# Kernel optimization log

Measured on AMD Instinct MI355X. Metric: run time of the kernel, lower is better.

Reference implementation:

```python
import jax, jax.numpy as jnp
import numpy as np

B = 8192        # batch
DB = 64         # dim_body
DO = 128        # dim_object
NOBJ = 9        # nb_objects (all connected)
NE = 72         # edges = NOBJ*(NOBJ-1)
DE = 128        # edge feature dim
NISO = 3        # isolated nodes
HID = 256
PHI_OUT = 256
ACT = 32
LOG_SIG_MIN, LOG_SIG_MAX = -20.0, 2.0


def setup_inputs() -> dict:
    key = jax.random.key(0)
    ks = jax.random.split(key, 16)
    s = 0.05
    return {
        "obs": jax.random.normal(ks[0], (B, DB + NOBJ * DO), jnp.float32),
        "edge_features": jax.random.normal(ks[1], (B, NE, DE), jnp.float32),
        # every object id 0..8 appears NE//NOBJ times (static edge targets)
        "edges_to": jnp.tile(jnp.arange(NOBJ, dtype=jnp.int32), NE // NOBJ),
        "isolated_nodes": jax.random.normal(ks[2], (B, NISO, DO), jnp.float32),
        "isolated_nodes_features": jax.random.normal(ks[3], (B, NISO, DE), jnp.float32),
        "W1_phi": jax.random.normal(ks[4], (DB + DO + DE, HID), jnp.float32) * s,
        "b1_phi": jnp.zeros((HID,), jnp.float32),
        "W2_phi": jax.random.normal(ks[5], (HID, PHI_OUT), jnp.float32) * s,
        "b2_phi": jnp.zeros((PHI_OUT,), jnp.float32),
        "W1_rho": jax.random.normal(ks[6], (PHI_OUT, HID), jnp.float32) * s,
        "b1_rho": jnp.zeros((HID,), jnp.float32),
        "Wm": jax.random.normal(ks[7], (HID, ACT), jnp.float32) * s,
        "bm": jnp.zeros((ACT,), jnp.float32),
        "Ws": jax.random.normal(ks[8], (HID, ACT), jnp.float32) * s,
        "bs": jnp.zeros((ACT,), jnp.float32),
    }


def reference(obs, edge_features, edges_to, isolated_nodes, isolated_nodes_features,
              W1_phi, b1_phi, W2_phi, b2_phi, W1_rho, b1_rho, Wm, bm, Ws, bs):
    obs_body = obs[:, :DB]                              # [B, DB]
    obs_objects = obs[:, DB:].reshape(B, NOBJ, DO)      # [B, NOBJ, DO]

    # per-node max over incoming edges (segment-max over static edge targets)
    ef = jnp.transpose(edge_features, (1, 0, 2))        # [NE, B, DE]
    incoming = jax.ops.segment_max(ef, edges_to, num_segments=NOBJ)  # [NOBJ, B, DE]

    body_c = jnp.broadcast_to(obs_body, (NOBJ, B, DB))
    inp_connected = jnp.concatenate(
        [body_c, jnp.transpose(obs_objects, (1, 0, 2)), incoming], axis=-1)

    body_i = jnp.broadcast_to(obs_body, (NISO, B, DB))
    inp_isolated = jnp.concatenate(
        [body_i,
         jnp.transpose(isolated_nodes, (1, 0, 2)),
         jnp.transpose(isolated_nodes_features, (1, 0, 2))], axis=-1)

    inp = jnp.concatenate([inp_connected, inp_isolated], axis=0)  # [NOBJ+NISO, B, DB+DO+DE]

    # phi DeepSet MLP
    h = jax.nn.relu(inp @ W1_phi + b1_phi)
    phi = jax.nn.relu(h @ W2_phi + b2_phi)

    pooled = phi.sum(axis=0)                            # readout='sum' -> [B, PHI_OUT]

    # rho MLP -> (mean, log_std)
    r = jax.nn.relu(pooled @ W1_rho + b1_rho)
    mean = r @ Wm + bm
    log_std = jnp.clip(r @ Ws + bs, LOG_SIG_MIN, LOG_SIG_MAX)
    return mean, log_std
```

## Files before the change

### kernel.cpp

```cpp
#include <hip/hip_runtime.h>
#include <hip/hip_bf16.h>
#include <stdint.h>


#define Bsz   8192
#define OBSW  1216
#define NH    256

typedef unsigned short u16;
typedef unsigned int   u32;

using bf16x8 = __attribute__((ext_vector_type(8))) short;
using f32x4  = __attribute__((ext_vector_type(4))) float;

__device__ u16   g_W1t[256 * 320];
__device__ u16   g_W2t[256 * 256];
__device__ u16   g_Rt [256 * 256];
__device__ u16   g_Wcat[64 * 256];
__device__ float g_pool2[2][Bsz * NH];

__device__ __forceinline__ u16 f2bf(float f) {
  union { float f; u32 i; } v; v.f = f;
  u32 x = v.i;
  x += 0x7fffu + ((x >> 16) & 1u);
  return (u16)(x >> 16);
}
__device__ __forceinline__ uint4 pack8(const float* f) {
  uint4 o;
  o.x = (u32)f2bf(f[0]) | ((u32)f2bf(f[1]) << 16);
  o.y = (u32)f2bf(f[2]) | ((u32)f2bf(f[3]) << 16);
  o.z = (u32)f2bf(f[4]) | ((u32)f2bf(f[5]) << 16);
  o.w = (u32)f2bf(f[6]) | ((u32)f2bf(f[7]) << 16);
  return o;
}
__device__ __forceinline__ void load8f(const float* p, float* f) {
  *(float4*)(f)     = *(const float4*)(p);
  *(float4*)(f + 4) = *(const float4*)(p + 4);
}

__global__ void transpose_cast(const float* __restrict__ in, int dst,
                               int K, int N, int row_off) {
  __shared__ u16 tile[32][33];
  u16* out = (dst == 0) ? g_W1t : (dst == 1) ? g_W2t : (dst == 2) ? g_Rt : g_Wcat;
  int k0 = blockIdx.x * 32, n0 = blockIdx.y * 32;
  int c = threadIdx.x & 31, r0 = threadIdx.x >> 5;
  #pragma unroll
  for (int i = 0; i < 4; i++) {
    int r = r0 + i * 8;
    tile[r][c] = f2bf(in[(size_t)(k0 + r) * N + (n0 + c)]);
  }
  __syncthreads();
  #pragma unroll
  for (int i = 0; i < 4; i++) {
    int r = r0 + i * 8;
    out[(size_t)(n0 + r + row_off) * K + (k0 + c)] = tile[c][r];
  }
}

__device__ __forceinline__ void loadA(
    int n, size_t sb, int sck,
    const float* __restrict__ obs, const float* __restrict__ ef,
    const float* __restrict__ iso, const float* __restrict__ isof,
    float f[4][8]) {
  if (n < 9) {
    const float* po = obs + sb * OBSW + 64 + (size_t)n * 128 + sck;
    load8f(po, f[0]);
    load8f(po + 64, f[1]);
    const float* base = ef + (sb * 72 + n) * 128 + sck;
    load8f(base, f[2]);
    load8f(base + 64, f[3]);
    #pragma unroll
    for (int j = 1; j < 8; j++) {
      float w0[8], w1[8];
      load8f(base + (size_t)j * 1152, w0);
      load8f(base + (size_t)j * 1152 + 64, w1);
      #pragma unroll
      for (int q = 0; q < 8; q++) {
        f[2][q] = fmaxf(f[2][q], w0[q]);
        f[3][q] = fmaxf(f[3][q], w1[q]);
      }
    }
  } else {
    const float* pi = iso  + (sb * 3 + (n - 9)) * 128 + sck;
    const float* pg = isof + (sb * 3 + (n - 9)) * 128 + sck;
    load8f(pi, f[0]); load8f(pi + 64, f[1]);
    load8f(pg, f[2]); load8f(pg + 64, f[3]);
  }
}

__global__ __launch_bounds__(256, 2)
void node_kernel(const float* __restrict__ obs, const float* __restrict__ ef,
                 const float* __restrict__ iso, const float* __restrict__ isof,
                 const float* __restrict__ b1, const float* __restrict__ b2) {
  __shared__ __attribute__((aligned(16))) u16 As[32][328];
  __shared__ __attribute__((aligned(16))) u16 Ht[32][264];
  const int btile = blockIdx.x >> 1;
  const int nhalf = blockIdx.x & 1;
  const int b0 = btile * 32;
  const int tid = threadIdx.x;
  const int wave = tid >> 6, lane = tid & 63;
  const int nw = wave * 64, lrow = lane & 15, quad = lane >> 4;
  const int srow = tid >> 3, sck = (tid & 7) * 8;
  const size_t sb = (size_t)(b0 + srow);

  {
    float fb[8];
    load8f(obs + sb * OBSW + sck, fb);
    *(uint4*)(&As[srow][sck]) = pack8(fb);
    float f[4][8];
    loadA(nhalf * 6, sb, sck, obs, ef, iso, isof, f);
    #pragma unroll
    for (int c = 0; c < 4; c++)
      *(uint4*)(&As[srow][(c + 1) * 64 + sck]) = pack8(f[c]);
  }
  __syncthreads();

  const f32x4 vzero = {0.f, 0.f, 0.f, 0.f};
  f32x4 pool[2][4];
  #pragma unroll
  for (int a = 0; a < 2; a++)
    #pragma unroll
    for (int b = 0; b < 4; b++) pool[a][b] = vzero;

  for (int nn = 0; nn < 6; nn++) {
    const int n = nhalf * 6 + nn;
    f32x4 acc[2][4];
    #pragma unroll
    for (int a = 0; a < 2; a++)
      #pragma unroll
      for (int b = 0; b < 4; b++) acc[a][b] = vzero;

    #pragma unroll
    for (int kc = 0; kc < 10; kc++) {
      const int kk = kc * 32 + quad * 8;
      bf16x8 af0 = *(const bf16x8*)(&As[lrow][kk]);
      bf16x8 af1 = *(const bf16x8*)(&As[16 + lrow][kk]);
      #pragma unroll
      for (int nb = 0; nb < 4; nb++) {
        bf16x8 bq = *(const bf16x8*)(g_W1t + (size_t)(nw + nb * 16 + lrow) * 320 + kk);
        acc[0][nb] = __builtin_amdgcn_mfma_f32_16x16x32_bf16(af0, bq, acc[0][nb], 0, 0, 0);
        acc[1][nb] = __builtin_amdgcn_mfma_f32_16x16x32_bf16(af1, bq, acc[1][nb], 0, 0, 0);
      }
    }

    float fnext[4][8];
    if (nn < 5) loadA(n + 1, sb, sck, obs, ef, iso, isof, fnext);

    #pragma unroll
    for (int nb = 0; nb < 4; nb++) {
      int col = nw + nb * 16 + lrow;
      float bv = b1[col];
      #pragma unroll
      for (int mb = 0; mb < 2; mb++)
        #pragma unroll
        for (int i = 0; i < 4; i++)
          Ht[mb * 16 + quad * 4 + i][col] = f2bf(fmaxf(acc[mb][nb][i] + bv, 0.f));
    }
    __syncthreads();

    if (nn < 5) {
      #pragma unroll
      for (int c = 0; c < 4; c++)
        *(uint4*)(&As[srow][(c + 1) * 64 + sck]) = pack8(fnext[c]);
    }

    #pragma unroll
    for (int a = 0; a < 2; a++)
      #pragma unroll
      for (int b = 0; b < 4; b++) acc[a][b] = vzero;

    #pragma unroll
    for (int kc = 0; kc < 8; kc++) {
      const int kk = kc * 32 + quad * 8;
      bf16x8 af0 = *(const bf16x8*)(&Ht[lrow][kk]);
      bf16x8 af1 = *(const bf16x8*)(&Ht[16 + lrow][kk]);
      #pragma unroll
      for (int nb = 0; nb < 4; nb++) {
        bf16x8 bq = *(const bf16x8*)(g_W2t + (size_t)(nw + nb * 16 + lrow) * 256 + kk);
        acc[0][nb] = __builtin_amdgcn_mfma_f32_16x16x32_bf16(af0, bq, acc[0][nb], 0, 0, 0);
        acc[1][nb] = __builtin_amdgcn_mfma_f32_16x16x32_bf16(af1, bq, acc[1][nb], 0, 0, 0);
      }
    }
    #pragma unroll
    for (int nb = 0; nb < 4; nb++) {
      int col = nw + nb * 16 + lrow;
      float bv = b2[col];
      #pragma unroll
      for (int mb = 0; mb < 2; mb++)
        #pragma unroll
        for (int i = 0; i < 4; i++)
          pool[mb][nb][i] += fmaxf(acc[mb][nb][i] + bv, 0.f);
    }
    __syncthreads();
  }

  float* op = g_pool2[nhalf];
  #pragma unroll
  for (int nb = 0; nb < 4; nb++) {
    int col = nw + nb * 16 + lrow;
    #pragma unroll
    for (int mb = 0; mb < 2; mb++)
      #pragma unroll
      for (int i = 0; i < 4; i++) {
        int row = b0 + mb * 16 + quad * 4 + i;
        op[(size_t)row * NH + col] = pool[mb][nb][i];
      }
  }
}

__global__ __launch_bounds__(256)
void rho_heads(const float* __restrict__ br, const float* __restrict__ bm,
               const float* __restrict__ bs, float* __restrict__ out) {
  __shared__ __attribute__((aligned(16))) u16 As2[32][264];
  const int b0 = blockIdx.x * 32;
  const int tid = threadIdx.x;
  const int wave = tid >> 6, lane = tid & 63;
  const int nw = wave * 64, lrow = lane & 15, quad = lane >> 4;
  const int srow = tid >> 3, sck = (tid & 7) * 8;

  #pragma unroll
  for (int c4 = 0; c4 < 4; c4++) {
    int col = c4 * 64 + sck;
    float f0[8], f1[8];
    load8f(g_pool2[0] + (size_t)(b0 + srow) * NH + col, f0);
    load8f(g_pool2[1] + (size_t)(b0 + srow) * NH + col, f1);
    #pragma unroll
    for (int q = 0; q < 8; q++) f0[q] += f1[q];
    *(uint4*)(&As2[srow][col]) = pack8(f0);
  }
  __syncthreads();

  const f32x4 vzero = {0.f, 0.f, 0.f, 0.f};
  f32x4 acc[2][4];
  #pragma unroll
  for (int a = 0; a < 2; a++)
    #pragma unroll
    for (int b = 0; b < 4; b++) acc[a][b] = vzero;

  #pragma unroll
  for (int kc = 0; kc < 8; kc++) {
    const int kk = kc * 32 + quad * 8;
    bf16x8 af0 = *(const bf16x8*)(&As2[lrow][kk]);
    bf16x8 af1 = *(const bf16x8*)(&As2[16 + lrow][kk]);
    #pragma unroll
    for (int nb = 0; nb < 4; nb++) {
      bf16x8 bq = *(const bf16x8*)(g_Rt + (size_t)(nw + nb * 16 + lrow) * 256 + kk);
      acc[0][nb] = __builtin_amdgcn_mfma_f32_16x16x32_bf16(af0, bq, acc[0][nb], 0, 0, 0);
      acc[1][nb] = __builtin_amdgcn_mfma_f32_16x16x32_bf16(af1, bq, acc[1][nb], 0, 0, 0);
    }
  }
  __syncthreads();

  #pragma unroll
  for (int nb = 0; nb < 4; nb++) {
    int col = nw + nb * 16 + lrow;
    float bv = br[col];
    #pragma unroll
    for (int mb = 0; mb < 2; mb++)
      #pragma unroll
      for (int i = 0; i < 4; i++)
        As2[mb * 16 + quad * 4 + i][col] = f2bf(fmaxf(acc[mb][nb][i] + bv, 0.f));
  }
  __syncthreads();

  f32x4 acc2[2] = {vzero, vzero};
  #pragma unroll
  for (int kc = 0; kc < 8; kc++) {
    const int kk = kc * 32 + quad * 8;
    bf16x8 af0 = *(const bf16x8*)(&As2[lrow][kk]);
    bf16x8 af1 = *(const bf16x8*)(&As2[16 + lrow][kk]);
    bf16x8 bq  = *(const bf16x8*)(g_Wcat + (size_t)(wave * 16 + lrow) * 256 + kk);
    acc2[0] = __builtin_amdgcn_mfma_f32_16x16x32_bf16(af0, bq, acc2[0], 0, 0, 0);
    acc2[1] = __builtin_amdgcn_mfma_f32_16x16x32_bf16(af1, bq, acc2[1], 0, 0, 0);
  }

  int j = wave * 16 + lrow;
  #pragma unroll
  for (int mb = 0; mb < 2; mb++) {
    #pragma unroll
    for (int i = 0; i < 4; i++) {
      int b = b0 + mb * 16 + quad * 4 + i;
      if (j < 32) {
        out[(size_t)b * 32 + j] = acc2[mb][i] + bm[j];
      } else {
        float v = acc2[mb][i] + bs[j - 32];
        v = fminf(fmaxf(v, -20.f), 2.f);
        out[(size_t)Bsz * 32 + (size_t)b * 32 + (j - 32)] = v;
      }
    }
  }
}

extern "C" void kernel_launch(void* const* d_in, const int* in_sizes, int n_in,
                              void* d_out, int out_size, void* d_ws, size_t ws_size,
                              hipStream_t stream) {
  const float* obs  = (const float*)d_in[0];
  const float* ef   = (const float*)d_in[1];
  const float* iso  = (const float*)d_in[3];
  const float* isof = (const float*)d_in[4];
  const float* W1   = (const float*)d_in[5];
  const float* b1   = (const float*)d_in[6];
  const float* W2   = (const float*)d_in[7];
  const float* b2   = (const float*)d_in[8];
  const float* Wr   = (const float*)d_in[9];
  const float* br   = (const float*)d_in[10];
  const float* Wm   = (const float*)d_in[11];
  const float* bm   = (const float*)d_in[12];
  const float* Wsg  = (const float*)d_in[13];
  const float* bs   = (const float*)d_in[14];
  float* out = (float*)d_out;
  (void)d_ws; (void)ws_size;

  transpose_cast<<<dim3(10, 8), 256, 0, stream>>>(W1, 0, 320, 256, 0);
  transpose_cast<<<dim3(8, 8), 256, 0, stream>>>(W2, 1, 256, 256, 0);
  transpose_cast<<<dim3(8, 8), 256, 0, stream>>>(Wr, 2, 256, 256, 0);
  transpose_cast<<<dim3(8, 1), 256, 0, stream>>>(Wm, 3, 256, 32, 0);
  transpose_cast<<<dim3(8, 1), 256, 0, stream>>>(Wsg, 3, 256, 32, 32);

  node_kernel<<<(Bsz / 32) * 2, 256, 0, stream>>>(obs, ef, iso, isof, b1, b2);
  rho_heads<<<Bsz / 32, 256, 0, stream>>>(br, bm, bs, out);
}
```

Baseline: 587.7 us.

## Halve batch tile to 16 rows, double-buffer node inputs, merge weight transposes

Shrinks the node kernel's batch tile from 32 to 16 rows, which doubles the block count and raises occupancy hints to 4 blocks per CU so more memory traffic can be in flight for the bandwidth-bound edge segment-max loads. It also double-buffers the A tile so the next node's inputs are written straight to LDS during the current node's compute, instead of being held in registers. The five weight-transpose launches are merged into one. In exchange, each block loads every W1/W2 B-fragment for half as many rows, doubling weight traffic from L2 per row, and each wave's MFMA work per fragment load is halved.

```diff
diff --git a/kernel.cpp b/kernel.cpp
--- a/kernel.cpp
+++ b/kernel.cpp
@@ -38,11 +38,18 @@
   *(float4*)(f + 4) = *(const float4*)(p + 4);
 }
 
-__global__ void transpose_cast(const float* __restrict__ in, int dst,
-                               int K, int N, int row_off) {
+__global__ __launch_bounds__(256)
+void transpose_all(const float* __restrict__ W1, const float* __restrict__ W2,
+                   const float* __restrict__ Wr, const float* __restrict__ Wm,
+                   const float* __restrict__ Wsg) {
   __shared__ u16 tile[32][33];
-  u16* out = (dst == 0) ? g_W1t : (dst == 1) ? g_W2t : (dst == 2) ? g_Rt : g_Wcat;
-  int k0 = blockIdx.x * 32, n0 = blockIdx.y * 32;
+  int bx = blockIdx.x;
+  const float* in; u16* out; int K, N, row_off = 0, k0, n0;
+  if (bx < 80)       { in = W1;  out = g_W1t;  K = 320; N = 256; k0 = (bx % 10) * 32; n0 = (bx / 10) * 32; }
+  else if (bx < 144) { bx -= 80;  in = W2;  out = g_W2t;  K = 256; N = 256; k0 = (bx & 7) * 32; n0 = (bx >> 3) * 32; }
+  else if (bx < 208) { bx -= 144; in = Wr;  out = g_Rt;   K = 256; N = 256; k0 = (bx & 7) * 32; n0 = (bx >> 3) * 32; }
+  else if (bx < 216) { bx -= 208; in = Wm;  out = g_Wcat; K = 256; N = 32;  k0 = bx * 32; n0 = 0; }
+  else               { bx -= 216; in = Wsg; out = g_Wcat; K = 256; N = 32;  k0 = bx * 32; n0 = 0; row_off = 32; }
   int c = threadIdx.x & 31, r0 = threadIdx.x >> 5;
   #pragma unroll
   for (int i = 0; i < 4; i++) {
@@ -57,128 +64,109 @@
   }
 }
 
-__device__ __forceinline__ void loadA(
-    int n, size_t sb, int sck,
+__device__ __forceinline__ void loadA16(
+    int n, size_t rb, int sck,
     const float* __restrict__ obs, const float* __restrict__ ef,
     const float* __restrict__ iso, const float* __restrict__ isof,
-    float f[4][8]) {
+    float f[2][8]) {
   if (n < 9) {
-    const float* po = obs + sb * OBSW + 64 + (size_t)n * 128 + sck;
-    load8f(po, f[0]);
-    load8f(po + 64, f[1]);
-    const float* base = ef + (sb * 72 + n) * 128 + sck;
-    load8f(base, f[2]);
-    load8f(base + 64, f[3]);
+    load8f(obs + rb * OBSW + 64 + (size_t)n * 128 + sck, f[0]);
+    const float* base = ef + (rb * 72 + n) * 128 + sck;
+    load8f(base, f[1]);
     #pragma unroll
     for (int j = 1; j < 8; j++) {
-      float w0[8], w1[8];
-      load8f(base + (size_t)j * 1152, w0);
-      load8f(base + (size_t)j * 1152 + 64, w1);
-      #pragma unroll
-      for (int q = 0; q < 8; q++) {
-        f[2][q] = fmaxf(f[2][q], w0[q]);
-        f[3][q] = fmaxf(f[3][q], w1[q]);
-      }
+      float w[8];
+      load8f(base + (size_t)j * 1152, w);
+      #pragma unroll
+      for (int q = 0; q < 8; q++) f[1][q] = fmaxf(f[1][q], w[q]);
     }
   } else {
-    const float* pi = iso  + (sb * 3 + (n - 9)) * 128 + sck;
-    const float* pg = isof + (sb * 3 + (n - 9)) * 128 + sck;
-    load8f(pi, f[0]); load8f(pi + 64, f[1]);
-    load8f(pg, f[2]); load8f(pg + 64, f[3]);
-  }
-}
-
-__global__ __launch_bounds__(256, 2)
+    load8f(iso  + (rb * 3 + (n - 9)) * 128 + sck, f[0]);
+    load8f(isof + (rb * 3 + (n - 9)) * 128 + sck, f[1]);
+  }
+}
+
+__global__ __launch_bounds__(256, 4)
 void node_kernel(const float* __restrict__ obs, const float* __restrict__ ef,
                  const float* __restrict__ iso, const float* __restrict__ isof,
                  const float* __restrict__ b1, const float* __restrict__ b2) {
-  __shared__ __attribute__((aligned(16))) u16 As[32][328];
-  __shared__ __attribute__((aligned(16))) u16 Ht[32][264];
+  __shared__ __attribute__((aligned(16))) u16 As[2][16][328];
+  __shared__ __attribute__((aligned(16))) u16 Ht[16][264];
   const int btile = blockIdx.x >> 1;
   const int nhalf = blockIdx.x & 1;
-  const int b0 = btile * 32;
+  const int b0 = btile * 16;
   const int tid = threadIdx.x;
   const int wave = tid >> 6, lane = tid & 63;
   const int nw = wave * 64, lrow = lane & 15, quad = lane >> 4;
-  const int srow = tid >> 3, sck = (tid & 7) * 8;
-  const size_t sb = (size_t)(b0 + srow);
+  const int trow = tid >> 4, sck = (tid & 15) * 8;
+  const size_t rb = (size_t)(b0 + trow);
 
   {
-    float fb[8];
-    load8f(obs + sb * OBSW + sck, fb);
-    *(uint4*)(&As[srow][sck]) = pack8(fb);
-    float f[4][8];
-    loadA(nhalf * 6, sb, sck, obs, ef, iso, isof, f);
-    #pragma unroll
-    for (int c = 0; c < 4; c++)
-      *(uint4*)(&As[srow][(c + 1) * 64 + sck]) = pack8(f[c]);
+    if (sck < 64) {
+      float fb[8];
+      load8f(obs + rb * OBSW + sck, fb);
+      uint4 p = pack8(fb);
+      *(uint4*)(&As[0][trow][sck]) = p;
+      *(uint4*)(&As[1][trow][sck]) = p;
+    }
+    float f[2][8];
+    loadA16(nhalf * 6, rb, sck, obs, ef, iso, isof, f);
+    *(uint4*)(&As[0][trow][64  + sck]) = pack8(f[0]);
+    *(uint4*)(&As[0][trow][192 + sck]) = pack8(f[1]);
   }
   __syncthreads();
 
   const f32x4 vzero = {0.f, 0.f, 0.f, 0.f};
-  f32x4 pool[2][4];
-  #pragma unroll
-  for (int a = 0; a < 2; a++)
-    #pragma unroll
-    for (int b = 0; b < 4; b++) pool[a][b] = vzero;
-
+  f32x4 pool[4];
+  #pragma unroll
+  for (int b = 0; b < 4; b++) pool[b] = vzero;
+
+  int cur = 0;
   for (int nn = 0; nn < 6; nn++) {
     const int n = nhalf * 6 + nn;
-    f32x4 acc[2][4];
-    #pragma unroll
-    for (int a = 0; a < 2; a++)
-      #pragma unroll
-      for (int b = 0; b < 4; b++) acc[a][b] = vzero;
+    f32x4 acc[4];
+    #pragma unroll
+    for (int b = 0; b < 4; b++) acc[b] = vzero;
 
     #pragma unroll
     for (int kc = 0; kc < 10; kc++) {
       const int kk = kc * 32 + quad * 8;
-      bf16x8 af0 = *(const bf16x8*)(&As[lrow][kk]);
-      bf16x8 af1 = *(const bf16x8*)(&As[16 + lrow][kk]);
+      bf16x8 af = *(const bf16x8*)(&As[cur][lrow][kk]);
       #pragma unroll
       for (int nb = 0; nb < 4; nb++) {
         bf16x8 bq = *(const bf16x8*)(g_W1t + (size_t)(nw + nb * 16 + lrow) * 320 + kk);
-        acc[0][nb] = __builtin_amdgcn_mfma_f32_16x16x32_bf16(af0, bq, acc[0][nb], 0, 0, 0);
-        acc[1][nb] = __builtin_amdgcn_mfma_f32_16x16x32_bf16(af1, bq, acc[1][nb], 0, 0, 0);
+        acc[nb] = __builtin_amdgcn_mfma_f32_16x16x32_bf16(af, bq, acc[nb], 0, 0, 0);
       }
     }
 
-    float fnext[4][8];
-    if (nn < 5) loadA(n + 1, sb, sck, obs, ef, iso, isof, fnext);
+    if (nn < 5) {
+      float f[2][8];
+      loadA16(n + 1, rb, sck, obs, ef, iso, isof, f);
+      *(uint4*)(&As[cur ^ 1][trow][64  + sck]) = pack8(f[0]);
+      *(uint4*)(&As[cur ^ 1][trow][192 + sck]) = pack8(f[1]);
+    }
 
     #pragma unroll
     for (int nb = 0; nb < 4; nb++) {
       int col = nw + nb * 16 + lrow;
       float bv = b1[col];
       #pragma unroll
-      for (int mb = 0; mb < 2; mb++)
-        #pragma unroll
-        for (int i = 0; i < 4; i++)
-          Ht[mb * 16 + quad * 4 + i][col] = f2bf(fmaxf(acc[mb][nb][i] + bv, 0.f));
+      for (int i = 0; i < 4; i++)
+        Ht[quad * 4 + i][col] = f2bf(fmaxf(acc[nb][i] + bv, 0.f));
     }
     __syncthreads();
 
-    if (nn < 5) {
-      #pragma unroll
-      for (int c = 0; c < 4; c++)
-        *(uint4*)(&As[srow][(c + 1) * 64 + sck]) = pack8(fnext[c]);
-    }
-
-    #pragma unroll
-    for (int a = 0; a < 2; a++)
-      #pragma unroll
-      for (int b = 0; b < 4; b++) acc[a][b] = vzero;
+    #pragma unroll
+    for (int b = 0; b < 4; b++) acc[b] = vzero;
 
     #pragma unroll
     for (int kc = 0; kc < 8; kc++) {
       const int kk = kc * 32 + quad * 8;
-      bf16x8 af0 = *(const bf16x8*)(&Ht[lrow][kk]);
-      bf16x8 af1 = *(const bf16x8*)(&Ht[16 + lrow][kk]);
+      bf16x8 af = *(const bf16x8*)(&Ht[lrow][kk]);
       #pragma unroll
       for (int nb = 0; nb < 4; nb++) {
         bf16x8 bq = *(const bf16x8*)(g_W2t + (size_t)(nw + nb * 16 + lrow) * 256 + kk);
-        acc[0][nb] = __builtin_amdgcn_mfma_f32_16x16x32_bf16(af0, bq, acc[0][nb], 0, 0, 0);
-        acc[1][nb] = __builtin_amdgcn_mfma_f32_16x16x32_bf16(af1, bq, acc[1][nb], 0, 0, 0);
+        acc[nb] = __builtin_amdgcn_mfma_f32_16x16x32_bf16(af, bq, acc[nb], 0, 0, 0);
       }
     }
     #pragma unroll
@@ -186,12 +174,11 @@
       int col = nw + nb * 16 + lrow;
       float bv = b2[col];
       #pragma unroll
-      for (int mb = 0; mb < 2; mb++)
-        #pragma unroll
-        for (int i = 0; i < 4; i++)
-          pool[mb][nb][i] += fmaxf(acc[mb][nb][i] + bv, 0.f);
+      for (int i = 0; i < 4; i++)
+        pool[nb][i] += fmaxf(acc[nb][i] + bv, 0.f);
     }
     __syncthreads();
+    cur ^= 1;
   }
 
   float* op = g_pool2[nhalf];
@@ -199,54 +186,48 @@
   for (int nb = 0; nb < 4; nb++) {
     int col = nw + nb * 16 + lrow;
     #pragma unroll
-    for (int mb = 0; mb < 2; mb++)
-      #pragma unroll
-      for (int i = 0; i < 4; i++) {
-        int row = b0 + mb * 16 + quad * 4 + i;
-        op[(size_t)row * NH + col] = pool[mb][nb][i];
-      }
-  }
-}
-
-__global__ __launch_bounds__(256)
+    for (int i = 0; i < 4; i++) {
+      int row = b0 + quad * 4 + i;
+      op[(size_t)row * NH + col] = pool[nb][i];
+    }
+  }
+}
+
+__global__ __launch_bounds__(256, 4)
 void rho_heads(const float* __restrict__ br, const float* __restrict__ bm,
                const float* __restrict__ bs, float* __restrict__ out) {
-  __shared__ __attribute__((aligned(16))) u16 As2[32][264];
-  const int b0 = blockIdx.x * 32;
+  __shared__ __attribute__((aligned(16))) u16 As2[16][264];
+  const int b0 = blockIdx.x * 16;
   const int tid = threadIdx.x;
   const int wave = tid >> 6, lane = tid & 63;
   const int nw = wave * 64, lrow = lane & 15, quad = lane >> 4;
-  const int srow = tid >> 3, sck = (tid & 7) * 8;
-
-  #pragma unroll
-  for (int c4 = 0; c4 < 4; c4++) {
-    int col = c4 * 64 + sck;
+  const int trow = tid >> 4, tcol = tid & 15;
+
+  #pragma unroll
+  for (int h = 0; h < 2; h++) {
+    int col = tcol * 16 + h * 8;
     float f0[8], f1[8];
-    load8f(g_pool2[0] + (size_t)(b0 + srow) * NH + col, f0);
-    load8f(g_pool2[1] + (size_t)(b0 + srow) * NH + col, f1);
+    load8f(g_pool2[0] + (size_t)(b0 + trow) * NH + col, f0);
+    load8f(g_pool2[1] + (size_t)(b0 + trow) * NH + col, f1);
     #pragma unroll
     for (int q = 0; q < 8; q++) f0[q] += f1[q];
-    *(uint4*)(&As2[srow][col]) = pack8(f0);
+    *(uint4*)(&As2[trow][col]) = pack8(f0);
   }
   __syncthreads();
 
   const f32x4 vzero = {0.f, 0.f, 0.f, 0.f};
-  f32x4 acc[2][4];
-  #pragma unroll
-  for (int a = 0; a < 2; a++)
-    #pragma unroll
-    for (int b = 0; b < 4; b++) acc[a][b] = vzero;
+  f32x4 acc[4];
+  #pragma unroll
+  for (int b = 0; b < 4; b++) acc[b] = vzero;
 
   #pragma unroll
   for (int kc = 0; kc < 8; kc++) {
     const int kk = kc * 32 + quad * 8;
-    bf16x8 af0 = *(const bf16x8*)(&As2[lrow][kk]);
-    bf16x8 af1 = *(const bf16x8*)(&As2[16 + lrow][kk]);
+    bf16x8 af = *(const bf16x8*)(&As2[lrow][kk]);
     #pragma unroll
     for (int nb = 0; nb < 4; nb++) {
       bf16x8 bq = *(const bf16x8*)(g_Rt + (size_t)(nw + nb * 16 + lrow) * 256 + kk);
-      acc[0][nb] = __builtin_amdgcn_mfma_f32_16x16x32_bf16(af0, bq, acc[0][nb], 0, 0, 0);
-      acc[1][nb] = __builtin_amdgcn_mfma_f32_16x16x32_bf16(af1, bq, acc[1][nb], 0, 0, 0);
+      acc[nb] = __builtin_amdgcn_mfma_f32_16x16x32_bf16(af, bq, acc[nb], 0, 0, 0);
     }
   }
   __syncthreads();
@@ -256,37 +237,30 @@
     int col = nw + nb * 16 + lrow;
     float bv = br[col];
     #pragma unroll
-    for (int mb = 0; mb < 2; mb++)
-      #pragma unroll
-      for (int i = 0; i < 4; i++)
-        As2[mb * 16 + quad * 4 + i][col] = f2bf(fmaxf(acc[mb][nb][i] + bv, 0.f));
-  }
-  __syncthreads();
-
-  f32x4 acc2[2] = {vzero, vzero};
+    for (int i = 0; i < 4; i++)
+      As2[quad * 4 + i][col] = f2bf(fmaxf(acc[nb][i] + bv, 0.f));
+  }
+  __syncthreads();
+
+  f32x4 acc2 = vzero;
   #pragma unroll
   for (int kc = 0; kc < 8; kc++) {
     const int kk = kc * 32 + quad * 8;
-    bf16x8 af0 = *(const bf16x8*)(&As2[lrow][kk]);
-    bf16x8 af1 = *(const bf16x8*)(&As2[16 + lrow][kk]);
-    bf16x8 bq  = *(const bf16x8*)(g_Wcat + (size_t)(wave * 16 + lrow) * 256 + kk);
-    acc2[0] = __builtin_amdgcn_mfma_f32_16x16x32_bf16(af0, bq, acc2[0], 0, 0, 0);
-    acc2[1] = __builtin_amdgcn_mfma_f32_16x16x32_bf16(af1, bq, acc2[1], 0, 0, 0);
+    bf16x8 af = *(const bf16x8*)(&As2[lrow][kk]);
+    bf16x8 bq = *(const bf16x8*)(g_Wcat + (size_t)(wave * 16 + lrow) * 256 + kk);
+    acc2 = __builtin_amdgcn_mfma_f32_16x16x32_bf16(af, bq, acc2, 0, 0, 0);
   }
 
   int j = wave * 16 + lrow;
   #pragma unroll
-  for (int mb = 0; mb < 2; mb++) {
-    #pragma unroll
-    for (int i = 0; i < 4; i++) {
-      int b = b0 + mb * 16 + quad * 4 + i;
-      if (j < 32) {
-        out[(size_t)b * 32 + j] = acc2[mb][i] + bm[j];
-      } else {
-        float v = acc2[mb][i] + bs[j - 32];
-        v = fminf(fmaxf(v, -20.f), 2.f);
-        out[(size_t)Bsz * 32 + (size_t)b * 32 + (j - 32)] = v;
-      }
+  for (int i = 0; i < 4; i++) {
+    int b = b0 + quad * 4 + i;
+    if (j < 32) {
+      out[(size_t)b * 32 + j] = acc2[i] + bm[j];
+    } else {
+      float v = acc2[i] + bs[j - 32];
+      v = fminf(fmaxf(v, -20.f), 2.f);
+      out[(size_t)Bsz * 32 + (size_t)b * 32 + (j - 32)] = v;
     }
   }
 }
@@ -311,12 +285,7 @@
   float* out = (float*)d_out;
   (void)d_ws; (void)ws_size;
 
-  transpose_cast<<<dim3(10, 8), 256, 0, stream>>>(W1, 0, 320, 256, 0);
-  transpose_cast<<<dim3(8, 8), 256, 0, stream>>>(W2, 1, 256, 256, 0);
-  transpose_cast<<<dim3(8, 8), 256, 0, stream>>>(Wr, 2, 256, 256, 0);
-  transpose_cast<<<dim3(8, 1), 256, 0, stream>>>(Wm, 3, 256, 32, 0);
-  transpose_cast<<<dim3(8, 1), 256, 0, stream>>>(Wsg, 3, 256, 32, 32);
-
-  node_kernel<<<(Bsz / 32) * 2, 256, 0, stream>>>(obs, ef, iso, isof, b1, b2);
-  rho_heads<<<Bsz / 32, 256, 0, stream>>>(br, bm, bs, out);
-}
+  transpose_all<<<224, 256, 0, stream>>>(W1, W2, Wr, Wm, Wsg);
+  node_kernel<<<(Bsz / 16) * 2, 256, 0, stream>>>(obs, ef, iso, isof, b1, b2);
+  rho_heads<<<Bsz / 16, 256, 0, stream>>>(br, bm, bs, out);
+}
```

Result: slower. 660.3 us (+12.4%).
